# Performance work log

Measured on AMD Instinct MI355X. Metric: run time of the kernel, lower is better.

The kernel has to match this reference:

```python
import jax, jax.numpy as jnp
import numpy as np

N = 50000        # num nodes
E = 800000       # num edges (avg degree 16)
IN = 64          # in_channels
H = 128          # hidden_channels
C1 = 64          # Num_TCN (fine clusters)
C2 = 16          # Num_TCN2 (coarse clusters)
DROP = 0.5       # drop_rate
THRESH = 1.0 / (C1 - 1)  # default edge_pruning_threshold
LN_EPS = 1e-5


def layer_norm(x, g, b):
    mu = jnp.mean(x, axis=-1, keepdims=True)
    var = jnp.var(x, axis=-1, keepdims=True)
    return (x - mu) * jax.lax.rsqrt(var + LN_EPS) * g + b


def graph_conv(x_src, row, col, W_rel, b, W_root, num_nodes):
    # PyG GraphConv (aggr='add'): out = lin_rel(sum_{src->dst} x[src]) + lin_root(x)
    agg = jax.ops.segment_sum(x_src[row], col, num_segments=num_nodes)
    return agg @ W_rel.T + b + x_src @ W_root.T


def mincut_common(x, s, A_s, deg):
    # shared tail of sparse_mincut_pool given A_s = A @ s and degree vector
    C = s.shape[-1]
    pooled_x = s.T @ x                                   # [C, F]
    pooled_adj = s.T @ A_s                               # [C, C]
    mincut_num = jnp.trace(pooled_adj)
    mincut_den = jnp.trace(s.T @ (deg[:, None] * s)) + 1e-10
    mincut_loss = -mincut_num / mincut_den
    sTs = s.T @ s
    norm = jnp.linalg.norm(sTs)
    ortho_loss = jnp.linalg.norm(sTs / (norm + 1e-10) - jnp.eye(C, dtype=x.dtype) / jnp.sqrt(jnp.asarray(C, x.dtype)))
    adj = pooled_adj * (1.0 - jnp.eye(C, dtype=x.dtype))  # fill_diagonal_(0)
    d_sqrt_inv = 1.0 / (jnp.sqrt(adj.sum(axis=1)) + 1e-15)
    adj_norm = adj * d_sqrt_inv[:, None] * d_sqrt_inv[None, :]
    return pooled_x, adj_norm, mincut_loss, ortho_loss


def mincut_sparse(x, row, col, s_logits, num_nodes):
    s = jax.nn.softmax(s_logits, axis=-1)
    # A_s[row] += s[col]  (edge_weight = 1) -> [N, C] scatter-add
    A_s = jax.ops.segment_sum(s[col], row, num_segments=num_nodes)
    deg = jax.ops.segment_sum(jnp.ones((row.shape[0],), x.dtype), row, num_segments=num_nodes)
    return mincut_common(x, s, A_s, deg)


def mincut_dense(x, M, s_logits):
    # pooled graph: dense 0/1 adjacency M[i,j]; equivalent to edge list from nonzero(M)
    s = jax.nn.softmax(s_logits, axis=-1)
    A_s = M @ s
    deg = M.sum(axis=1)
    return mincut_common(x, s, A_s, deg)


def setup_inputs() -> dict:
    key = jax.random.key(0)
    ks = jax.random.split(key, 12)
    x = jax.random.normal(ks[0], (N, IN), jnp.float32)
    edge_index = jax.random.randint(ks[1], (2, E), 0, N, jnp.int32)
    # bernoulli(1 - drop_rate) node-drop mask, fixed for determinism
    drop_mask = (jax.random.uniform(ks[2], (N,)) > DROP).astype(jnp.float32)
    p = lambda k, shp: (jax.random.normal(k, shp, jnp.float32) * 0.05)
    return dict(
        x=x, edge_index=edge_index, drop_mask=drop_mask,
        W1_rel=p(ks[3], (H, IN)), b1=jnp.zeros((H,), jnp.float32), W1_root=p(ks[4], (H, IN)),
        pW1=p(ks[5], (C1, H)), pb1=jnp.zeros((C1,), jnp.float32),
        g1=jnp.ones((C1,), jnp.float32), be1=jnp.zeros((C1,), jnp.float32),
        W2_rel=p(ks[6], (H, H)), b2=jnp.zeros((H,), jnp.float32), W2_root=p(ks[7], (H, H)),
        pW2=p(ks[8], (C2, H)), pb2=jnp.zeros((C2,), jnp.float32),
        g2=jnp.ones((C2,), jnp.float32), be2=jnp.zeros((C2,), jnp.float32),
    )


def reference(x, edge_index, drop_mask, W1_rel, b1, W1_root, pW1, pb1, g1, be1,
              W2_rel, b2, W2_root, pW2, pb2, g2, be2):
    # training=True path, S=1 (loss sums / S are identity)
    row, col = edge_index[0], edge_index[1]
    x_drop = drop_mask[:, None] * x
    x1 = jax.nn.relu(graph_conv(x_drop, row, col, W1_rel, b1, W1_root, N))   # [N, H]
    s1 = layer_norm(x1 @ pW1.T + pb1, g1, be1)                               # [N, C1]
    ls1 = jax.nn.log_softmax(s1, axis=-1)
    x_pool1, adj_pool1, mc1, o1 = mincut_sparse(x1, row, col, s1, N)
    # edge pruning -> dense 0/1 pooled adjacency (replaces nonzero + edge list)
    M = jnp.where(adj_pool1 > THRESH, 1.0, 0.0).astype(x.dtype)              # [C1, C1]
    # GraphConv on pooled graph: aggregate x[src] at dst == M.T @ x_pool1
    x2 = jax.nn.relu((M.T @ x_pool1) @ W2_rel.T + b2 + x_pool1 @ W2_root.T)  # [C1, H]
    s2 = layer_norm(x2 @ pW2.T + pb2, g2, be2)                               # [C1, C2]
    ls2 = jax.nn.log_softmax(s2, axis=-1)
    _, _, mc2, o2 = mincut_dense(x2, M, s2)
    return (mc1, o1, mc2, o2, ls1, ls2)
```

## Files before the change

kernel.cpp:

```cpp
#include <hip/hip_runtime.h>
#include <hip/hip_bf16.h>

#define NN 50000
#define NE 800000
#define INC 64
#define HC 128
#define NC1 64
#define NC2 16
#define DCAP 64

#define OFF_FLAG 0
#define OFW_W1R 16
#define OFW_W1O 8208
#define OFW_B1  16400
#define OFW_PW1 16528
#define OFW_PB1 24720
#define OFW_G1  24784
#define OFW_BE1 24848
#define OFW_W2R 24912
#define OFW_B2  41296
#define OFW_W2O 41424
#define OFW_PW2 57808
#define OFW_PB2 59856
#define OFW_G2  59872
#define OFW_BE2 59888
#define CVT_TOTAL 59888

#define OFW_PW1T 59904
#define OFF_MG   68096
#define OFF_MTG  72192
#define OFF_DEG2 76288
#define OFF_S2G  76352
#define OFF_XD   127792
#define OFF_X1   3327792
#define OFF_S    9727792
#define OFF_AGG  12927792
#define OFF_CSRC 16127792
#define OFF_SCAL 17727792
#define OFF_PX   17727808
#define OFF_PADJ 17736000
#define OFF_STS  17740096
#define OFF_CUR  17744192
#define OFF_Q    17794192
#define OFF_END  17844192
#define ZERO_FLOATS (OFF_END - OFF_SCAL)

#define OFF_PXSTSP OFF_XD
#define OFF_PADJP  OFF_X1
#define P_POOL 256
#define P_PADJ 1024
#define XSS 132

__device__ inline float bflo(unsigned int u){ return __uint_as_float(u << 16); }
__device__ inline float bfhi(unsigned int u){ return __uint_as_float(u & 0xffff0000u); }

__device__ inline float wave_sum(float v){
#pragma unroll
  for (int o = 32; o > 0; o >>= 1) v += __shfl_xor(v, o, 64);
  return v;
}

__device__ inline void store_out(void* out, long long idx, float v, bool bf){
  if (bf) ((__hip_bfloat16*)out)[idx] = __float2bfloat16(v);
  else    ((float*)out)[idx] = v;
}

__device__ inline float block_reduce_256(float v, float* red, int t){
  red[t] = v; __syncthreads();
#pragma unroll
  for (int sh = 128; sh > 0; sh >>= 1){
    if (t < sh) red[t] += red[t + sh];
    __syncthreads();
  }
  float r = red[0];
  __syncthreads();
  return r;
}

__global__ void k_detect(const unsigned int* __restrict__ dmw, float* __restrict__ flag){
  __shared__ int cnt;
  if (threadIdx.x == 0) cnt = 0;
  __syncthreads();
  int c = 0;
  for (int i = threadIdx.x; i < 12288; i += 256){
    unsigned int w = dmw[i];
    if (w == 0x3F803F80u || w == 0x00003F80u) c++;
  }
  atomicAdd(&cnt, c);
  __syncthreads();
  if (threadIdx.x == 0) flag[0] = (cnt > 64) ? 1.0f : 0.0f;
}

__global__ void k_cvt(const void* p0, const void* p1, const void* p2, const void* p3,
                      const void* p4, const void* p5, const void* p6, const void* p7,
                      const void* p8, const void* p9, const void* p10, const void* p11,
                      const void* p12, const void* p13,
                      const float* __restrict__ flag, float* __restrict__ ws){
  int i = blockIdx.x * blockDim.x + threadIdx.x;
  if (i >= CVT_TOTAL) return;
  const void* src; int off;
  if      (i < 8192 ){ src = p0;  off = i; }
  else if (i < 16384){ src = p1;  off = i - 8192; }
  else if (i < 16512){ src = p2;  off = i - 16384; }
  else if (i < 24704){ src = p3;  off = i - 16512; }
  else if (i < 24768){ src = p4;  off = i - 24704; }
  else if (i < 24832){ src = p5;  off = i - 24768; }
  else if (i < 24896){ src = p6;  off = i - 24832; }
  else if (i < 41280){ src = p7;  off = i - 24896; }
  else if (i < 41408){ src = p8;  off = i - 41280; }
  else if (i < 57792){ src = p9;  off = i - 41408; }
  else if (i < 59840){ src = p10; off = i - 57792; }
  else if (i < 59856){ src = p11; off = i - 59840; }
  else if (i < 59872){ src = p12; off = i - 59856; }
  else               { src = p13; off = i - 59872; }
  float v = (flag[0] > 0.5f) ? __bfloat162float(((const __hip_bfloat16*)src)[off])
                             : ((const float*)src)[off];
  ws[16 + i] = v;
  if (i >= 16512 && i < 24704){
    int o2 = i - 16512;
    int c = o2 >> 7, k = o2 & 127;
    ws[OFW_PW1T + k * 64 + c] = v;
  }
}

__global__ void k_xdrop(const void* __restrict__ xr, const void* __restrict__ dmr,
                        const float* __restrict__ flag, float* __restrict__ xd){
  int i4 = blockIdx.x * blockDim.x + threadIdx.x;
  if (i4 >= NN * 16) return;
  int n = i4 >> 4;
  float4 o;
  if (flag[0] > 0.5f){
    uint2 w = ((const uint2*)xr)[i4];
    float dv = __bfloat162float(((const __hip_bfloat16*)dmr)[n]);
    o.x = bflo(w.x) * dv; o.y = bfhi(w.x) * dv;
    o.z = bflo(w.y) * dv; o.w = bfhi(w.y) * dv;
  } else {
    float4 xv = ((const float4*)xr)[i4];
    float dv = ((const float*)dmr)[n];
    o.x = xv.x * dv; o.y = xv.y * dv; o.z = xv.z * dv; o.w = xv.w * dv;
  }
  ((float4*)xd)[i4] = o;
}

__global__ void k_fillC(const int* __restrict__ ei, int* __restrict__ cur,
                        unsigned short* __restrict__ csrc2){
  int e = blockIdx.x * blockDim.x + threadIdx.x;
  if (e < NE){
    int r = ei[e], c = ei[NE + e];
    int pos = atomicAdd(&cur[c], 1);
    if (pos < DCAP) csrc2[(c << 6) + pos] = (unsigned short)r;
  }
}

__device__ inline float4 gather_rowsum16(const unsigned short* __restrict__ idxarr,
                                         int st, int en,
                                         const float* __restrict__ table, int lane,
                                         int g, int sub){
  float4 a0 = {0,0,0,0}, a1 = {0,0,0,0}, a2 = {0,0,0,0}, a3 = {0,0,0,0};
  for (int bb = st; bb < en; bb += 64){
    int rem = en - bb;
    int myi = (bb + lane < en) ? (int)idxarr[bb + lane] : 0;
    int niter = ((rem < 64 ? rem : 64) + 3) >> 2;
    int i = 0;
    for (; i + 4 <= niter; i += 4){
      int s0 = __shfl(myi, g + ((i    ) << 2), 64);
      int s1 = __shfl(myi, g + ((i + 1) << 2), 64);
      int s2 = __shfl(myi, g + ((i + 2) << 2), 64);
      int s3 = __shfl(myi, g + ((i + 3) << 2), 64);
      if ((g + (i << 2))       < rem){ float4 v = *(const float4*)(table + (s0 << 6) + (sub << 2)); a0.x += v.x; a0.y += v.y; a0.z += v.z; a0.w += v.w; }
      if ((g + ((i + 1) << 2)) < rem){ float4 v = *(const float4*)(table + (s1 << 6) + (sub << 2)); a1.x += v.x; a1.y += v.y; a1.z += v.z; a1.w += v.w; }
      if ((g + ((i + 2) << 2)) < rem){ float4 v = *(const float4*)(table + (s2 << 6) + (sub << 2)); a2.x += v.x; a2.y += v.y; a2.z += v.z; a2.w += v.w; }
      if ((g + ((i + 3) << 2)) < rem){ float4 v = *(const float4*)(table + (s3 << 6) + (sub << 2)); a3.x += v.x; a3.y += v.y; a3.z += v.z; a3.w += v.w; }
    }
    for (; i < niter; ++i){
      int slot = g + (i << 2);
      int s0 = __shfl(myi, slot, 64);
      if (slot < rem){ float4 v = *(const float4*)(table + (s0 << 6) + (sub << 2)); a0.x += v.x; a0.y += v.y; a0.z += v.z; a0.w += v.w; }
    }
  }
  float4 a;
  a.x = (a0.x + a1.x) + (a2.x + a3.x);
  a.y = (a0.y + a1.y) + (a2.y + a3.y);
  a.z = (a0.z + a1.z) + (a2.z + a3.z);
  a.w = (a0.w + a1.w) + (a2.w + a3.w);
  a.x += __shfl_xor(a.x, 16, 64); a.x += __shfl_xor(a.x, 32, 64);
  a.y += __shfl_xor(a.y, 16, 64); a.y += __shfl_xor(a.y, 32, 64);
  a.z += __shfl_xor(a.z, 16, 64); a.z += __shfl_xor(a.z, 32, 64);
  a.w += __shfl_xor(a.w, 16, 64); a.w += __shfl_xor(a.w, 32, 64);
  return a;
}

__global__ __launch_bounds__(256) void k_agg2(const int* __restrict__ cur,
                                              const unsigned short* __restrict__ csrc2,
                                              const float* __restrict__ xd,
                                              float* __restrict__ agg){
  int gid = blockIdx.x * 256 + threadIdx.x;
  int lane = gid & 63, wid = gid >> 6;
  int nw = (gridDim.x * 256) >> 6;
  int g = lane >> 4, sub = lane & 15;
  for (int n = wid; n < NN; n += nw){
    int c = cur[n]; if (c > DCAP) c = DCAP;
    int st = n << 6, en = st + c;
    float4 a = gather_rowsum16(csrc2, st, en, xd, lane, g, sub);
    if (g == 0) *(float4*)(agg + (n << 6) + (sub << 2)) = a;
  }
}

__global__ __launch_bounds__(128) void k_x1(const float* __restrict__ agg,
                                            const float* __restrict__ xd,
                                            const float* __restrict__ wts,
                                            float* __restrict__ x1){
  __shared__ float nb[8][2][64];
  int t = threadIdx.x;
  float wr[64], wo[64];
#pragma unroll
  for (int j = 0; j < 64; ++j){
    wr[j] = wts[OFW_W1R + t * 64 + j];
    wo[j] = wts[OFW_W1O + t * 64 + j];
  }
  float bias = wts[OFW_B1 + t];
  const int nbatch = NN / 8;
  for (int b = blockIdx.x; b < nbatch; b += gridDim.x){
    int base = b * 8;
#pragma unroll
    for (int i = 0; i < 2; ++i){
      int f = t + (i << 7);
      int u = f >> 5;
      int j = f & 31;
      const float* src = (j < 16) ? (agg + ((base + u) << 6) + (j << 2))
                                  : (xd  + ((base + u) << 6) + ((j - 16) << 2));
      *(float4*)&nb[u][j >> 4][(j & 15) << 2] = *(const float4*)src;
    }
    __syncthreads();
#pragma unroll
    for (int u = 0; u < 8; ++u){
      float acc_a = bias, acc_x = 0.0f;
#pragma unroll
      for (int j = 0; j < 16; ++j){
        float4 va = *(const float4*)&nb[u][0][j << 2];
        float4 vx = *(const float4*)&nb[u][1][j << 2];
        acc_a += va.x * wr[4*j] + va.y * wr[4*j+1] + va.z * wr[4*j+2] + va.w * wr[4*j+3];
        acc_x += vx.x * wo[4*j] + vx.y * wo[4*j+1] + vx.z * wo[4*j+2] + vx.w * wo[4*j+3];
      }
      x1[(base + u) * HC + t] = fmaxf(acc_a + acc_x, 0.0f);
    }
    __syncthreads();
  }
}

__global__ __launch_bounds__(256) void k_s1f(const float* __restrict__ x1,
                                             const float* __restrict__ wts,
                                             float* __restrict__ s,
                                             float* __restrict__ q,
                                             void* __restrict__ outp,
                                             const float* __restrict__ flag){
  __shared__ float xs[64 * XSS];
  __shared__ float pwc[64 * 64];
  __shared__ float gsh[64], bsh[64];
  int t = threadIdx.x;
  int base = blockIdx.x * 64;
  if (t < 64){ gsh[t] = wts[OFW_G1 + t]; bsh[t] = wts[OFW_BE1 + t]; }
  for (int f = t; f < 64 * 32; f += 256){
    int r = f >> 5, kq = f & 31;
    float4 v = (base + r < NN) ? *(const float4*)(x1 + (base + r) * HC + (kq << 2))
                               : make_float4(0, 0, 0, 0);
    *(float4*)&xs[r * XSS + (kq << 2)] = v;
  }
  int ni = t >> 4, cj = t & 15;
  float4 c0 = {0,0,0,0}, c1 = {0,0,0,0}, c2 = {0,0,0,0}, c3 = {0,0,0,0};
#pragma unroll
  for (int half = 0; half < 2; ++half){
    int k0 = half << 6;
    __syncthreads();
    for (int f = t; f < 1024; f += 256){
      int kk = f >> 4, qq = f & 15;
      *(float4*)&pwc[kk * 64 + (qq << 2)] =
          *(const float4*)&wts[OFW_PW1T + (k0 + kk) * 64 + (qq << 2)];
    }
    __syncthreads();
    for (int kk = 0; kk < 64; kk += 4){
      float4 a0 = *(const float4*)&xs[(ni * 4 + 0) * XSS + k0 + kk];
      float4 a1 = *(const float4*)&xs[(ni * 4 + 1) * XSS + k0 + kk];
      float4 a2 = *(const float4*)&xs[(ni * 4 + 2) * XSS + k0 + kk];
      float4 a3 = *(const float4*)&xs[(ni * 4 + 3) * XSS + k0 + kk];
      float4 b0 = *(const float4*)&pwc[(kk + 0) * 64 + (cj << 2)];
      float4 b1 = *(const float4*)&pwc[(kk + 1) * 64 + (cj << 2)];
      float4 b2 = *(const float4*)&pwc[(kk + 2) * 64 + (cj << 2)];
      float4 b3 = *(const float4*)&pwc[(kk + 3) * 64 + (cj << 2)];
      c0.x += a0.x*b0.x + a0.y*b1.x + a0.z*b2.x + a0.w*b3.x;
      c0.y += a0.x*b0.y + a0.y*b1.y + a0.z*b2.y + a0.w*b3.y;
      c0.z += a0.x*b0.z + a0.y*b1.z + a0.z*b2.z + a0.w*b3.z;
      c0.w += a0.x*b0.w + a0.y*b1.w + a0.z*b2.w + a0.w*b3.w;
      c1.x += a1.x*b0.x + a1.y*b1.x + a1.z*b2.x + a1.w*b3.x;
      c1.y += a1.x*b0.y + a1.y*b1.y + a1.z*b2.y + a1.w*b3.y;
      c1.z += a1.x*b0.z + a1.y*b1.z + a1.z*b2.z + a1.w*b3.z;
      c1.w += a1.x*b0.w + a1.y*b1.w + a1.z*b2.w + a1.w*b3.w;
      c2.x += a2.x*b0.x + a2.y*b1.x + a2.z*b2.x + a2.w*b3.x;
      c2.y += a2.x*b0.y + a2.y*b1.y + a2.z*b2.y + a2.w*b3.y;
      c2.z += a2.x*b0.z + a2.y*b1.z + a2.z*b2.z + a2.w*b3.z;
      c2.w += a2.x*b0.w + a2.y*b1.w + a2.z*b2.w + a2.w*b3.w;
      c3.x += a3.x*b0.x + a3.y*b1.x + a3.z*b2.x + a3.w*b3.x;
      c3.y += a3.x*b0.y + a3.y*b1.y + a3.z*b2.y + a3.w*b3.y;
      c3.z += a3.x*b0.z + a3.y*b1.z + a3.z*b2.z + a3.w*b3.z;
      c3.w += a3.x*b0.w + a3.y*b1.w + a3.z*b2.w + a3.w*b3.w;
    }
  }
  float4 pb = *(const float4*)&wts[OFW_PB1 + (cj << 2)];
  c0.x += pb.x; c0.y += pb.y; c0.z += pb.z; c0.w += pb.w;
  c1.x += pb.x; c1.y += pb.y; c1.z += pb.z; c1.w += pb.w;
  c2.x += pb.x; c2.y += pb.y; c2.z += pb.z; c2.w += pb.w;
  c3.x += pb.x; c3.y += pb.y; c3.z += pb.z; c3.w += pb.w;
  __syncthreads();
  *(float4*)&xs[(ni * 4 + 0) * XSS + (cj << 2)] = c0;
  *(float4*)&xs[(ni * 4 + 1) * XSS + (cj << 2)] = c1;
  *(float4*)&xs[(ni * 4 + 2) * XSS + (cj << 2)] = c2;
  *(float4*)&xs[(ni * 4 + 3) * XSS + (cj << 2)] = c3;
  __syncthreads();
  bool bf = flag[0] > 0.5f;
  int lane = t & 63, wv = t >> 6;
  float gl = gsh[lane], bl = bsh[lane];
  for (int rb = 0; rb < 16; rb += 4){
    int row = wv * 16 + rb;
    float z0 = xs[(row + 0) * XSS + lane];
    float z1 = xs[(row + 1) * XSS + lane];
    float z2 = xs[(row + 2) * XSS + lane];
    float z3 = xs[(row + 3) * XSS + lane];
    float s0 = z0, s1 = z1, s2 = z2, s3 = z3;
    float q0 = z0*z0, q1 = z1*z1, q2 = z2*z2, q3 = z3*z3;
#pragma unroll
    for (int o = 32; o > 0; o >>= 1){
      s0 += __shfl_xor(s0, o, 64); q0 += __shfl_xor(q0, o, 64);
      s1 += __shfl_xor(s1, o, 64); q1 += __shfl_xor(q1, o, 64);
      s2 += __shfl_xor(s2, o, 64); q2 += __shfl_xor(q2, o, 64);
      s3 += __shfl_xor(s3, o, 64); q3 += __shfl_xor(q3, o, 64);
    }
    float mu0 = s0 * 0.015625f, mu1 = s1 * 0.015625f;
    float mu2 = s2 * 0.015625f, mu3 = s3 * 0.015625f;
    float va0 = q0 * 0.015625f - mu0 * mu0;
    float va1 = q1 * 0.015625f - mu1 * mu1;
    float va2 = q2 * 0.015625f - mu2 * mu2;
    float va3 = q3 * 0.015625f - mu3 * mu3;
    float y0 = (z0 - mu0) * rsqrtf(va0 + 1e-5f) * gl + bl;
    float y1 = (z1 - mu1) * rsqrtf(va1 + 1e-5f) * gl + bl;
    float y2 = (z2 - mu2) * rsqrtf(va2 + 1e-5f) * gl + bl;
    float y3 = (z3 - mu3) * rsqrtf(va3 + 1e-5f) * gl + bl;
    float m0 = y0, m1 = y1, m2 = y2, m3 = y3;
#pragma unroll
    for (int o = 32; o > 0; o >>= 1){
      m0 = fmaxf(m0, __shfl_xor(m0, o, 64));
      m1 = fmaxf(m1, __shfl_xor(m1, o, 64));
      m2 = fmaxf(m2, __shfl_xor(m2, o, 64));
      m3 = fmaxf(m3, __shfl_xor(m3, o, 64));
    }
    float e0 = expf(y0 - m0), e1 = expf(y1 - m1);
    float e2 = expf(y2 - m2), e3 = expf(y3 - m3);
    float u0 = e0, u1 = e1, u2 = e2, u3 = e3;
    float w0 = e0*e0, w1 = e1*e1, w2 = e2*e2, w3 = e3*e3;
#pragma unroll
    for (int o = 32; o > 0; o >>= 1){
      u0 += __shfl_xor(u0, o, 64); w0 += __shfl_xor(w0, o, 64);
      u1 += __shfl_xor(u1, o, 64); w1 += __shfl_xor(w1, o, 64);
      u2 += __shfl_xor(u2, o, 64); w2 += __shfl_xor(w2, o, 64);
      u3 += __shfl_xor(u3, o, 64); w3 += __shfl_xor(w3, o, 64);
    }
    int n0 = base + row;
    if (n0 + 0 < NN){ s[(n0 + 0) * 64 + lane] = e0 / u0;
      store_out(outp, 4LL + (long long)(n0 + 0) * 64 + lane, (y0 - m0) - logf(u0), bf);
      if (lane == 0) q[n0 + 0] = w0 / (u0 * u0); }
    if (n0 + 1 < NN){ s[(n0 + 1) * 64 + lane] = e1 / u1;
      store_out(outp, 4LL + (long long)(n0 + 1) * 64 + lane, (y1 - m1) - logf(u1), bf);
      if (lane == 0) q[n0 + 1] = w1 / (u1 * u1); }
    if (n0 + 2 < NN){ s[(n0 + 2) * 64 + lane] = e2 / u2;
      store_out(outp, 4LL + (long long)(n0 + 2) * 64 + lane, (y2 - m2) - logf(u2), bf);
      if (lane == 0) q[n0 + 2] = w2 / (u2 * u2); }
    if (n0 + 3 < NN){ s[(n0 + 3) * 64 + lane] = e3 / u3;
      store_out(outp, 4LL + (long long)(n0 + 3) * 64 + lane, (y3 - m3) - logf(u3), bf);
      if (lane == 0) q[n0 + 3] = w3 / (u3 * u3); }
  }
}

__global__ __launch_bounds__(256) void k_den(const int* __restrict__ ei,
                                             const float* __restrict__ q,
                                             float* __restrict__ scal){
  __shared__ float red[256];
  int t = threadIdx.x;
  float acc = 0.0f;
  for (int e = blockIdx.x * 256 + t; e < NE; e += gridDim.x * 256)
    acc += q[ei[e]];
  float r = block_reduce_256(acc, red, t);
  if (t == 0) atomicAdd(&scal[0], r);
}

__global__ __launch_bounds__(256) void k_padj2(const int* __restrict__ cur,
                                               const unsigned short* __restrict__ csrc2,
                                               const float* __restrict__ s,
                                               float* __restrict__ padjp){
  __shared__ float rs[16 * 64];
  __shared__ float ra[16 * 64];
  int t = threadIdx.x, lane = t & 63, w = t >> 6;
  int g = lane >> 4, sub = lane & 15;
  int i4 = t >> 4;
  int j4 = t & 15;
  float4 acc0 = {0,0,0,0}, acc1 = {0,0,0,0}, acc2 = {0,0,0,0}, acc3 = {0,0,0,0};
  const int nbatch = NN / 16;
  for (int b = blockIdx.x; b < nbatch; b += gridDim.x){
    int base = b * 16;
#pragma unroll
    for (int qq = 0; qq < 4; ++qq){
      int k = w * 4 + qq;
      int n = base + k;
      int c = cur[n]; if (c > DCAP) c = DCAP;
      int st = n << 6, en = st + c;
      float4 a = gather_rowsum16(csrc2, st, en, s, lane, g, sub);
      if (g == 0){
        *(float4*)&rs[k * 64 + (sub << 2)] = a;
      } else if (g == 1){
        *(float4*)&ra[k * 64 + (sub << 2)] = *(const float4*)(s + (n << 6) + (sub << 2));
      }
    }
    __syncthreads();
#pragma unroll
    for (int k = 0; k < 16; ++k){
      float4 a  = *(const float4*)&rs[k * 64 + (i4 << 2)];
      float4 bv = *(const float4*)&ra[k * 64 + (j4 << 2)];
      acc0.x += a.x * bv.x; acc0.y += a.x * bv.y; acc0.z += a.x * bv.z; acc0.w += a.x * bv.w;
      acc1.x += a.y * bv.x; acc1.y += a.y * bv.y; acc1.z += a.y * bv.z; acc1.w += a.y * bv.w;
      acc2.x += a.z * bv.x; acc2.y += a.z * bv.y; acc2.z += a.z * bv.z; acc2.w += a.z * bv.w;
      acc3.x += a.w * bv.x; acc3.y += a.w * bv.y; acc3.z += a.w * bv.z; acc3.w += a.w * bv.w;
    }
    __syncthreads();
  }
  float* pp = padjp + blockIdx.x * 4096;
  *(float4*)&pp[(i4 * 4 + 0) * 64 + (j4 << 2)] = acc0;
  *(float4*)&pp[(i4 * 4 + 1) * 64 + (j4 << 2)] = acc1;
  *(float4*)&pp[(i4 * 4 + 2) * 64 + (j4 << 2)] = acc2;
  *(float4*)&pp[(i4 * 4 + 3) * 64 + (j4 << 2)] = acc3;
}

__global__ __launch_bounds__(1024) void k_pool(const float* __restrict__ s,
                                               const float* __restrict__ x1,
                                               float* __restrict__ part){
  __shared__ float ssh[32 * 64];
  __shared__ float xsh[32 * 128];
  int t = threadIdx.x;
  int c = t >> 4, q = t & 15;
  float4 apx0 = {0,0,0,0}, apx1 = {0,0,0,0}, ast0 = {0,0,0,0};
  const int nbatch = (NN + 31) / 32;
  for (int b = blockIdx.x; b < nbatch; b += gridDim.x){
    int base = b * 32;
    int kmax = NN - base; if (kmax > 32) kmax = 32;
    if (t < 512){
      int k = t >> 4, col = t & 15;
      float4 v = (k < kmax) ? *(const float4*)(s + ((base + k) << 6) + (col << 2))
                            : make_float4(0, 0, 0, 0);
      *(float4*)&ssh[k * 64 + (col << 2)] = v;
    }
    {
      int k = t >> 5, col = t & 31;
      float4 v = (k < kmax) ? *(const float4*)(x1 + (base + k) * HC + (col << 2))
                            : make_float4(0, 0, 0, 0);
      *(float4*)&xsh[k * 128 + (col << 2)] = v;
    }
    __syncthreads();
    for (int k = 0; k < kmax; ++k){
      float sv = ssh[k * 64 + c];
      float4 xv0 = *(const float4*)&xsh[k * 128 + (q << 2)];
      float4 xv1 = *(const float4*)&xsh[k * 128 + ((q + 16) << 2)];
      float4 s0  = *(const float4*)&ssh[k * 64 + (q << 2)];
      apx0.x += sv * xv0.x; apx0.y += sv * xv0.y; apx0.z += sv * xv0.z; apx0.w += sv * xv0.w;
      apx1.x += sv * xv1.x; apx1.y += sv * xv1.y; apx1.z += sv * xv1.z; apx1.w += sv * xv1.w;
      ast0.x += sv * s0.x;  ast0.y += sv * s0.y;  ast0.z += sv * s0.z;  ast0.w += sv * s0.w;
    }
    __syncthreads();
  }
  float* pp = part + blockIdx.x * 12288;
  *(float4*)&pp[c * 128 + (q << 2)]        = apx0;
  *(float4*)&pp[c * 128 + ((q + 16) << 2)] = apx1;
  *(float4*)&pp[8192 + c * 64 + (q << 2)]  = ast0;
}

__global__ __launch_bounds__(256) void k_red(const float* __restrict__ pxstsp,
                                             const float* __restrict__ padjp,
                                             float* __restrict__ px,
                                             float* __restrict__ sts,
                                             float* __restrict__ padj){
  __shared__ float sh[256];
  int b = blockIdx.x, t = threadIdx.x;
  int ci = t & 63, pc = t >> 6;
  if (b < 192){
    int cell = b * 64 + ci;
    float a0 = 0, a1 = 0, a2 = 0, a3 = 0;
    const float* basep = pxstsp + cell;
    int p0 = pc * (P_POOL / 4);
    for (int p = 0; p < P_POOL / 4; p += 4){
      a0 += basep[(p0 + p    ) * 12288];
      a1 += basep[(p0 + p + 1) * 12288];
      a2 += basep[(p0 + p + 2) * 12288];
      a3 += basep[(p0 + p + 3) * 12288];
    }
    sh[t] = (a0 + a1) + (a2 + a3);
    __syncthreads();
    if (t < 64){
      float r = sh[t] + sh[t + 64] + sh[t + 128] + sh[t + 192];
      int cell2 = b * 64 + t;
      if (cell2 < 8192) px[cell2] = r; else sts[cell2 - 8192] = r;
    }
  } else {
    int cell = (b - 192) * 64 + ci;
    float a0 = 0, a1 = 0, a2 = 0, a3 = 0;
    const float* basep = padjp + cell;
    int p0 = pc * (P_PADJ / 4);
    for (int p = 0; p < P_PADJ / 4; p += 4){
      a0 += basep[(p0 + p    ) * 4096];
      a1 += basep[(p0 + p + 1) * 4096];
      a2 += basep[(p0 + p + 2) * 4096];
      a3 += basep[(p0 + p + 3) * 4096];
    }
    sh[t] = (a0 + a1) + (a2 + a3);
    __syncthreads();
    if (t < 64) padj[(b - 192) * 64 + t] = sh[t] + sh[t + 64] + sh[t + 128] + sh[t + 192];
  }
}

__global__ __launch_bounds__(256) void k_m(const float* __restrict__ padj,
                                           const float* __restrict__ sts,
                                           float* __restrict__ Mg,
                                           float* __restrict__ Mtg,
                                           float* __restrict__ deg2,
                                           float* __restrict__ scal){
  __shared__ float red[256];
  __shared__ float psh[4096];
  __shared__ float dsi[64];
  int t = threadIdx.x;
  const float TH = 1.0f / 63.0f;
  for (int i = t; i < 4096; i += 256) psh[i] = padj[i];
  __syncthreads();
  float v = (t < 64) ? psh[t * 65] : 0.0f;
  float num1 = block_reduce_256(v, red, t);
  v = 0.0f;
  for (int i = t; i < 4096; i += 256){ float e = sts[i]; v += e * e; }
  float nrm1 = sqrtf(block_reduce_256(v, red, t));
  v = 0.0f;
  for (int i = t; i < 4096; i += 256){
    float e = sts[i] / (nrm1 + 1e-10f) - ((i % 65 == 0) ? 0.125f : 0.0f);
    v += e * e;
  }
  float o1 = sqrtf(block_reduce_256(v, red, t));
  if (t < 64){
    float rs = 0.0f;
    for (int j = 0; j < 64; ++j) rs += (j == t) ? 0.0f : psh[t * 64 + j];
    dsi[t] = 1.0f / (sqrtf(rs) + 1e-15f);
  }
  __syncthreads();
  for (int i = t; i < 4096; i += 256){
    int r = i >> 6, c = i & 63;
    float a = (r == c) ? 0.0f : psh[i];
    float m = (a * dsi[r] * dsi[c] > TH) ? 1.0f : 0.0f;
    Mg[i] = m;
    Mtg[c * 64 + r] = m;
  }
  __syncthreads();
  for (int i = t; i < 4096; i += 256){
    int r = i >> 6, c = i & 63;
    float a = (r == c) ? 0.0f : psh[i];
    psh[i] = (a * dsi[r] * dsi[c] > TH) ? 1.0f : 0.0f;
  }
  __syncthreads();
  if (t < 64){
    float d2 = 0.0f;
    for (int j = 0; j < 64; ++j) d2 += psh[t * 64 + j];
    deg2[t] = d2;
  }
  if (t == 0){ scal[1] = num1; scal[2] = o1; }
}

__global__ __launch_bounds__(128) void k_x2(const float* __restrict__ Mtg,
                                            const float* __restrict__ px,
                                            const float* __restrict__ wts,
                                            float* __restrict__ s2g,
                                            void* __restrict__ out,
                                            const float* __restrict__ flag){
  __shared__ float mt[64], pxc[128], mpsh[128], x2sh[128];
  __shared__ float part[16][9], lsh[16], stat[2];
  int c = blockIdx.x, t = threadIdx.x;
  if (t < 64) mt[t] = Mtg[c * 64 + t];
  pxc[t] = px[c * 128 + t];
  __syncthreads();
  float mp = 0.0f;
  for (int i = 0; i < 64; ++i) mp += mt[i] * px[i * 128 + t];
  mpsh[t] = mp;
  __syncthreads();
  float acc = wts[OFW_B2 + t];
  const float* wrr = wts + OFW_W2R + t * 128;
  const float* wor = wts + OFW_W2O + t * 128;
  for (int k = 0; k < 128; ++k) acc += mpsh[k] * wrr[k] + pxc[k] * wor[k];
  x2sh[t] = fmaxf(acc, 0.0f);
  __syncthreads();
  { int u = t >> 3, p = t & 7;
    const float* pw = wts + OFW_PW2 + u * 128 + p * 16;
    float pa = 0.0f;
    for (int k = 0; k < 16; ++k) pa += x2sh[p * 16 + k] * pw[k];
    part[u][p] = pa;
  }
  __syncthreads();
  if (t < 16){
    float l = wts[OFW_PB2 + t];
    for (int p = 0; p < 8; ++p) l += part[t][p];
    lsh[t] = l;
  }
  __syncthreads();
  if (t == 0){
    float mu = 0.0f;
    for (int u = 0; u < 16; ++u) mu += lsh[u];
    mu *= (1.0f / 16.0f);
    float var = 0.0f;
    for (int u = 0; u < 16; ++u){ float d = lsh[u] - mu; var += d * d; }
    var *= (1.0f / 16.0f);
    float rstd = rsqrtf(var + 1e-5f);
    float m = -3.4e38f;
    for (int u = 0; u < 16; ++u){
      lsh[u] = (lsh[u] - mu) * rstd * wts[OFW_G2 + u] + wts[OFW_BE2 + u];
      m = fmaxf(m, lsh[u]);
    }
    float se = 0.0f;
    for (int u = 0; u < 16; ++u) se += expf(lsh[u] - m);
    stat[0] = m; stat[1] = logf(se);
  }
  __syncthreads();
  if (t < 16){
    float ls = (lsh[t] - stat[0]) - stat[1];
    store_out(out, 4LL + (long long)NN * NC1 + c * 16 + t, ls, flag[0] > 0.5f);
    s2g[c * 16 + t] = expf(ls);
  }
}

__global__ __launch_bounds__(256) void k_tail(const float* __restrict__ Mg,
                                              const float* __restrict__ s2g,
                                              const float* __restrict__ deg2,
                                              const float* __restrict__ scal,
                                              void* __restrict__ out,
                                              const float* __restrict__ flag){
  __shared__ float red[256];
  __shared__ float Msh[4096];
  __shared__ float s2sh[1024];
  __shared__ float d2sh[64];
  __shared__ float sts2[256];
  int t = threadIdx.x;
  for (int i = t; i < 4096; i += 256) Msh[i] = Mg[i];
  for (int i = t; i < 1024; i += 256) s2sh[i] = s2g[i];
  if (t < 64) d2sh[t] = deg2[t];
  __syncthreads();
  float vnum = 0.0f, vden = 0.0f;
  for (int m = 0; m < 4; ++m){
    int id = t + m * 256;
    int c = id >> 4, u = id & 15;
    float a = 0.0f;
    for (int j = 0; j < 64; ++j) a += Msh[c * 64 + j] * s2sh[j * 16 + u];
    float sv = s2sh[id];
    vnum += sv * a;
    vden += d2sh[c] * sv * sv;
  }
  float num2 = block_reduce_256(vnum, red, t);
  float den2 = block_reduce_256(vden, red, t) + 1e-10f;
  { int u = t >> 4, w = t & 15;
    float a = 0.0f;
    for (int c2 = 0; c2 < 64; ++c2) a += s2sh[c2 * 16 + u] * s2sh[c2 * 16 + w];
    sts2[t] = a;
  }
  __syncthreads();
  float v = sts2[t] * sts2[t];
  float nrm2 = sqrtf(block_reduce_256(v, red, t));
  { float e = sts2[t] / (nrm2 + 1e-10f) - (((t >> 4) == (t & 15)) ? 0.25f : 0.0f);
    v = e * e; }
  float o2 = sqrtf(block_reduce_256(v, red, t));
  if (t == 0){
    bool bf = flag[0] > 0.5f;
    float den = scal[0] + 1e-10f;
    store_out(out, 0, -scal[1] / den, bf);
    store_out(out, 1, scal[2], bf);
    store_out(out, 2, -num2 / den2, bf);
    store_out(out, 3, o2, bf);
  }
}

extern "C" void kernel_launch(void* const* d_in, const int* in_sizes, int n_in,
                              void* d_out, int out_size, void* d_ws, size_t ws_size,
                              hipStream_t stream){
  const void* x  = d_in[0];
  const int*  ei = (const int*)d_in[1];
  const void* dm = d_in[2];

  float* ws    = (float*)d_ws;
  float* flag  = ws + OFF_FLAG;
  float* xd    = ws + OFF_XD;
  float* x1    = ws + OFF_X1;
  float* s     = ws + OFF_S;
  float* agg   = ws + OFF_AGG;
  float* px    = ws + OFF_PX;
  float* padj  = ws + OFF_PADJ;
  float* sts   = ws + OFF_STS;
  float* scal  = ws + OFF_SCAL;
  float* Mg    = ws + OFF_MG;
  float* Mtg   = ws + OFF_MTG;
  float* deg2  = ws + OFF_DEG2;
  float* s2g   = ws + OFF_S2G;
  float* q     = ws + OFF_Q;
  float* pxstsp= ws + OFF_PXSTSP;
  float* padjp = ws + OFF_PADJP;
  unsigned short* csrc2 = (unsigned short*)(ws + OFF_CSRC);
  int* cur = (int*)(ws + OFF_CUR);

  hipMemsetAsync(ws + OFF_SCAL, 0, (size_t)ZERO_FLOATS * sizeof(float), stream);

  k_detect<<<1, 256, 0, stream>>>((const unsigned int*)dm, flag);
  k_cvt<<<(CVT_TOTAL + 255) / 256, 256, 0, stream>>>(
      d_in[3], d_in[5], d_in[4], d_in[6], d_in[7], d_in[8], d_in[9],
      d_in[10], d_in[11], d_in[12], d_in[13], d_in[14], d_in[15], d_in[16],
      flag, ws);
  k_xdrop<<<(NN * 16 + 255) / 256, 256, 0, stream>>>(x, dm, flag, xd);
  k_fillC<<<(NE + 255) / 256, 256, 0, stream>>>(ei, cur, csrc2);
  k_agg2<<<2048, 256, 0, stream>>>(cur, csrc2, xd, agg);
  k_x1<<<2048, 128, 0, stream>>>(agg, xd, ws, x1);
  k_s1f<<<(NN + 63) / 64, 256, 0, stream>>>(x1, ws, s, q, d_out, flag);
  k_den<<<256, 256, 0, stream>>>(ei, q, scal);
  k_pool<<<P_POOL, 1024, 0, stream>>>(s, x1, pxstsp);
  k_padj2<<<P_PADJ, 256, 0, stream>>>(cur, csrc2, s, padjp);
  k_red<<<256, 256, 0, stream>>>(pxstsp, padjp, px, sts, padj);
  k_m<<<1, 256, 0, stream>>>(padj, sts, Mg, Mtg, deg2, scal);
  k_x2<<<64, 128, 0, stream>>>(Mtg, px, ws, s2g, d_out, flag);
  k_tail<<<1, 256, 0, stream>>>(Mg, s2g, deg2, scal, d_out, flag);
}
```

Measured before the change: 455.4 us.

## Rewrite first GraphConv linear as register-tiled GEMM with LDS-resident weights

k_cvt now also writes a transposed, concatenated [W1_rel; W1_root] matrix (128x128) into the workspace. k_x1 loads this matrix into shared memory once per block and stages a 64-node tile of [agg | x_drop] in LDS. Each of 512 threads then computes a 4-node by 4-channel output block with float4 loads and writes the biased ReLU output as float4. This replaces the old scheme of 128 per-thread register weights over 8-node batches, aiming for more reuse per LDS read and fewer tiny batches. The price is 96KB of LDS per block, which limits residency to one block per CU despite the launch bound of two.

```diff
diff --git a/kernel.cpp b/kernel.cpp
--- a/kernel.cpp
+++ b/kernel.cpp
@@ -31,6 +31,7 @@
 #define OFF_MTG  72192
 #define OFF_DEG2 76288
 #define OFF_S2G  76352
+#define OFW_WCT  77376
 #define OFF_XD   127792
 #define OFF_X1   3327792
 #define OFF_S    9727792
@@ -116,7 +117,14 @@
   float v = (flag[0] > 0.5f) ? __bfloat162float(((const __hip_bfloat16*)src)[off])
                              : ((const float*)src)[off];
   ws[16 + i] = v;
-  if (i >= 16512 && i < 24704){
+  if (i < 8192){
+    int h = i >> 6, j = i & 63;
+    ws[OFW_WCT + j * 128 + h] = v;
+  } else if (i < 16384){
+    int o2 = i - 8192;
+    int h = o2 >> 6, j = o2 & 63;
+    ws[OFW_WCT + (64 + j) * 128 + h] = v;
+  } else if (i >= 16512 && i < 24704){
     int o2 = i - 16512;
     int c = o2 >> 7, k = o2 & 127;
     ws[OFW_PW1T + k * 64 + c] = v;
@@ -206,45 +214,79 @@
   }
 }
 
-__global__ __launch_bounds__(128) void k_x1(const float* __restrict__ agg,
-                                            const float* __restrict__ xd,
-                                            const float* __restrict__ wts,
-                                            float* __restrict__ x1){
-  __shared__ float nb[8][2][64];
+#define FMA4(ACC, AV) \
+  ACC.x += AV.x*w0.x + AV.y*w1.x + AV.z*w2.x + AV.w*w3.x; \
+  ACC.y += AV.x*w0.y + AV.y*w1.y + AV.z*w2.y + AV.w*w3.y; \
+  ACC.z += AV.x*w0.z + AV.y*w1.z + AV.z*w2.z + AV.w*w3.z; \
+  ACC.w += AV.x*w0.w + AV.y*w1.w + AV.z*w2.w + AV.w*w3.w;
+
+__global__ __launch_bounds__(512, 2) void k_x1(const float* __restrict__ agg,
+                                               const float* __restrict__ xd,
+                                               const float* __restrict__ wts,
+                                               float* __restrict__ x1){
+  __shared__ __align__(16) float wt[128 * 128];
+  __shared__ __align__(16) float at[64 * 128];
   int t = threadIdx.x;
-  float wr[64], wo[64];
-#pragma unroll
-  for (int j = 0; j < 64; ++j){
-    wr[j] = wts[OFW_W1R + t * 64 + j];
-    wo[j] = wts[OFW_W1O + t * 64 + j];
-  }
-  float bias = wts[OFW_B1 + t];
-  const int nbatch = NN / 8;
-  for (int b = blockIdx.x; b < nbatch; b += gridDim.x){
-    int base = b * 8;
-#pragma unroll
-    for (int i = 0; i < 2; ++i){
-      int f = t + (i << 7);
-      int u = f >> 5;
-      int j = f & 31;
-      const float* src = (j < 16) ? (agg + ((base + u) << 6) + (j << 2))
-                                  : (xd  + ((base + u) << 6) + ((j - 16) << 2));
-      *(float4*)&nb[u][j >> 4][(j & 15) << 2] = *(const float4*)src;
-    }
-    __syncthreads();
-#pragma unroll
-    for (int u = 0; u < 8; ++u){
-      float acc_a = bias, acc_x = 0.0f;
-#pragma unroll
-      for (int j = 0; j < 16; ++j){
-        float4 va = *(const float4*)&nb[u][0][j << 2];
-        float4 vx = *(const float4*)&nb[u][1][j << 2];
-        acc_a += va.x * wr[4*j] + va.y * wr[4*j+1] + va.z * wr[4*j+2] + va.w * wr[4*j+3];
-        acc_x += vx.x * wo[4*j] + vx.y * wo[4*j+1] + vx.z * wo[4*j+2] + vx.w * wo[4*j+3];
+  for (int f4 = t; f4 < 4096; f4 += 512)
+    *(float4*)&wt[f4 << 2] = *(const float4*)&wts[OFW_WCT + (f4 << 2)];
+  int ni = t >> 5;
+  int cj = t & 31;
+  float4 b4 = *(const float4*)&wts[OFW_B1 + (cj << 2)];
+  const int ntiles = (NN + 63) >> 6;
+  for (int tile = blockIdx.x; tile < ntiles; tile += gridDim.x){
+    int base = tile << 6;
+    __syncthreads();
+    for (int f4 = t; f4 < 2048; f4 += 512){
+      int i = f4 >> 5, kq = f4 & 31;
+      int n = base + i;
+      float4 v = make_float4(0.f, 0.f, 0.f, 0.f);
+      if (n < NN){
+        int k = kq << 2;
+        v = (k < 64) ? *(const float4*)(agg + (n << 6) + k)
+                     : *(const float4*)(xd  + (n << 6) + (k - 64));
       }
-      x1[(base + u) * HC + t] = fmaxf(acc_a + acc_x, 0.0f);
-    }
-    __syncthreads();
+      *(float4*)&at[(i << 7) + (kq << 2)] = v;
+    }
+    __syncthreads();
+    float4 acc0 = {0,0,0,0}, acc1 = {0,0,0,0}, acc2 = {0,0,0,0}, acc3 = {0,0,0,0};
+    const float* ap = at + (ni << 9);
+    const float* wp = wt + (cj << 2);
+#pragma unroll 4
+    for (int k = 0; k < 128; k += 4){
+      float4 w0 = *(const float4*)(wp + ((k + 0) << 7));
+      float4 w1 = *(const float4*)(wp + ((k + 1) << 7));
+      float4 w2 = *(const float4*)(wp + ((k + 2) << 7));
+      float4 w3 = *(const float4*)(wp + ((k + 3) << 7));
+      float4 a0v = *(const float4*)(ap + k);
+      float4 a1v = *(const float4*)(ap + 128 + k);
+      float4 a2v = *(const float4*)(ap + 256 + k);
+      float4 a3v = *(const float4*)(ap + 384 + k);
+      FMA4(acc0, a0v)
+      FMA4(acc1, a1v)
+      FMA4(acc2, a2v)
+      FMA4(acc3, a3v)
+    }
+    int n0 = base + (ni << 2);
+    if (n0 + 0 < NN){
+      float4 o; o.x = fmaxf(acc0.x + b4.x, 0.f); o.y = fmaxf(acc0.y + b4.y, 0.f);
+      o.z = fmaxf(acc0.z + b4.z, 0.f); o.w = fmaxf(acc0.w + b4.w, 0.f);
+      *(float4*)(x1 + (long long)(n0 + 0) * HC + (cj << 2)) = o;
+    }
+    if (n0 + 1 < NN){
+      float4 o; o.x = fmaxf(acc1.x + b4.x, 0.f); o.y = fmaxf(acc1.y + b4.y, 0.f);
+      o.z = fmaxf(acc1.z + b4.z, 0.f); o.w = fmaxf(acc1.w + b4.w, 0.f);
+      *(float4*)(x1 + (long long)(n0 + 1) * HC + (cj << 2)) = o;
+    }
+    if (n0 + 2 < NN){
+      float4 o; o.x = fmaxf(acc2.x + b4.x, 0.f); o.y = fmaxf(acc2.y + b4.y, 0.f);
+      o.z = fmaxf(acc2.z + b4.z, 0.f); o.w = fmaxf(acc2.w + b4.w, 0.f);
+      *(float4*)(x1 + (long long)(n0 + 2) * HC + (cj << 2)) = o;
+    }
+    if (n0 + 3 < NN){
+      float4 o; o.x = fmaxf(acc3.x + b4.x, 0.f); o.y = fmaxf(acc3.y + b4.y, 0.f);
+      o.z = fmaxf(acc3.z + b4.z, 0.f); o.w = fmaxf(acc3.w + b4.w, 0.f);
+      *(float4*)(x1 + (long long)(n0 + 3) * HC + (cj << 2)) = o;
+    }
   }
 }
 
@@ -720,7 +762,7 @@
   k_xdrop<<<(NN * 16 + 255) / 256, 256, 0, stream>>>(x, dm, flag, xd);
   k_fillC<<<(NE + 255) / 256, 256, 0, stream>>>(ei, cur, csrc2);
   k_agg2<<<2048, 256, 0, stream>>>(cur, csrc2, xd, agg);
-  k_x1<<<2048, 128, 0, stream>>>(agg, xd, ws, x1);
+  k_x1<<<256, 512, 0, stream>>>(agg, xd, ws, x1);
   k_s1f<<<(NN + 63) / 64, 256, 0, stream>>>(x1, ws, s, q, d_out, flag);
   k_den<<<256, 256, 0, stream>>>(ei, q, scal);
   k_pool<<<P_POOL, 1024, 0, stream>>>(s, x1, pxstsp);
```

After: 435.9 us. -4.3%, faster.
